# Kernel optimization log

Measured on AMD Instinct MI355X. Metric: run time of the kernel, lower is better.

Reference implementation:

```python
import jax, jax.numpy as jnp
import numpy as np

N_NODES = 100000; N_EDGES = 800000
N_SVC = 51200; E_SVC = 409600
B = 1024; OUT = 50; HID = 128; EMB = 64; VOCAB = 100
BN_EPS = 1e-5


def _bn(x, g, b):
    # BatchNorm1d in training mode: biased batch statistics
    m = x.mean(0)
    v = x.var(0)
    return (x - m) * jax.lax.rsqrt(v + BN_EPS) * g + b


def _gin(x, ei, W1, b1, bng, bnb, W2, b2, eps, n):
    # GINConv: nn((1+eps)*x + sum_{j->i} x_j), aggregate source feats at target ei[1]
    agg = jax.ops.segment_sum(x[ei[0]], ei[1], num_segments=n)
    h = (1.0 + eps) * x + agg
    h = _bn(h @ W1 + b1, bng, bnb)
    return jax.nn.relu(h) @ W2 + b2


def _gcn(x, ei, ew, W, b, n):
    # GCNConv with edge weights: add self loops (w=1), symmetric normalization
    xw = x @ W
    loop = jnp.arange(n)
    row = jnp.concatenate([ei[0], loop])
    col = jnp.concatenate([ei[1], loop])
    w = jnp.concatenate([ew, jnp.ones((n,), ew.dtype)])
    deg = jax.ops.segment_sum(w, col, num_segments=n)
    dinv = jnp.where(deg > 0, jax.lax.rsqrt(deg), 0.0)
    norm = dinv[row] * w * dinv[col]
    return jax.ops.segment_sum(norm[:, None] * xw[row], col, num_segments=n) + b


def setup_inputs() -> dict:
    key = jax.random.key(0)
    ks = jax.random.split(key, 48)
    p = lambda k, s: jax.random.normal(k, s, jnp.float32) * 0.05
    H2 = 2 * HID
    inp = dict(
        node_ids=jax.random.randint(ks[0], (N_NODES,), 0, VOCAB),
        node_feats=jax.random.normal(ks[1], (N_NODES, 6), jnp.float32),
        edge_index=jax.random.randint(ks[2], (2, N_EDGES), 0, N_NODES),
        svc_ids=jax.random.randint(ks[3], (N_SVC,), 0, VOCAB),
        svc_feats=jax.random.normal(ks[4], (N_SVC, 4), jnp.float32),
        edge_index_service=jax.random.randint(ks[5], (2, E_SVC), 0, N_SVC),
        edge_attr_service=jax.random.uniform(ks[6], (E_SVC,), jnp.float32),
        batch=jnp.sort(jax.random.randint(ks[7], (N_NODES,), 0, B)),
        num_graphs=B,
        out_channels=OUT,
        emb_node=p(ks[8], (VOCAB, EMB)),
        emb_svc=p(ks[9], (VOCAB, EMB)),
        # GIN layer 0 (in = EMB + 6)
        g0_W1=p(ks[10], (EMB + 6, H2)), g0_b1=jnp.zeros((H2,), jnp.float32),
        g0_bng1=jnp.ones((H2,), jnp.float32), g0_bnb1=jnp.zeros((H2,), jnp.float32),
        g0_W2=p(ks[11], (H2, HID)), g0_b2=jnp.zeros((HID,), jnp.float32),
        g0_eps=jnp.zeros((), jnp.float32),
        bn0_g=jnp.ones((HID,), jnp.float32), bn0_b=jnp.zeros((HID,), jnp.float32),
        # GIN layer 1 (in = HID)
        g1_W1=p(ks[12], (HID, H2)), g1_b1=jnp.zeros((H2,), jnp.float32),
        g1_bng1=jnp.ones((H2,), jnp.float32), g1_bnb1=jnp.zeros((H2,), jnp.float32),
        g1_W2=p(ks[13], (H2, HID)), g1_b2=jnp.zeros((HID,), jnp.float32),
        g1_eps=jnp.zeros((), jnp.float32),
        bn1_g=jnp.ones((HID,), jnp.float32), bn1_b=jnp.zeros((HID,), jnp.float32),
        node_lin_W=p(ks[14], (HID, HID)), node_lin_b=jnp.zeros((HID,), jnp.float32),
        # GCN layer 0 (in = EMB + 4)
        c0_W=p(ks[15], (EMB + 4, H2)), c0_b=jnp.zeros((H2,), jnp.float32),
        cbn0_g=jnp.ones((H2,), jnp.float32), cbn0_b=jnp.zeros((H2,), jnp.float32),
        # GCN layer 1 (in = 2*HID)
        c1_W=p(ks[16], (H2, H2)), c1_b=jnp.zeros((H2,), jnp.float32),
        cbn1_g=jnp.ones((H2,), jnp.float32), cbn1_b=jnp.zeros((H2,), jnp.float32),
        svc_lin_W=p(ks[17], (H2, HID)), svc_lin_b=jnp.zeros((HID,), jnp.float32),
    )
    return inp


def reference(node_feats, svc_feats, edge_attr_service, emb_node, emb_svc,
              g0_W1, g0_b1, g0_bng1, g0_bnb1, g0_W2, g0_b2, g0_eps, bn0_g, bn0_b,
              g1_W1, g1_b1, g1_bng1, g1_bnb1, g1_W2, g1_b2, g1_eps, bn1_g, bn1_b,
              node_lin_W, node_lin_b,
              c0_W, c0_b, cbn0_g, cbn0_b, c1_W, c1_b, cbn1_g, cbn1_b,
              svc_lin_W, svc_lin_b,
              node_ids, svc_ids, edge_index, edge_index_service, batch,
              num_graphs, out_channels):
    n = node_feats.shape[0]
    ns = svc_feats.shape[0]
    # node branch: embedding(col 0) ++ 6 float cols, 2 GIN layers
    x = jnp.concatenate([emb_node[node_ids], node_feats], axis=-1)
    x = jax.nn.relu(_bn(_gin(x, edge_index, g0_W1, g0_b1, g0_bng1, g0_bnb1,
                             g0_W2, g0_b2, g0_eps, n), bn0_g, bn0_b))
    x = jax.nn.relu(_bn(_gin(x, edge_index, g1_W1, g1_b1, g1_bng1, g1_bnb1,
                             g1_W2, g1_b2, g1_eps, n), bn1_g, bn1_b))
    # service branch: embedding ++ 4 qos cols, 2 GCN layers (isServices=True)
    xs = jnp.concatenate([emb_svc[svc_ids], svc_feats], axis=-1)
    xs = jax.nn.relu(_bn(_gcn(xs, edge_index_service, edge_attr_service, c0_W, c0_b, ns),
                         cbn0_g, cbn0_b))
    xs = jax.nn.relu(_bn(_gcn(xs, edge_index_service, edge_attr_service, c1_W, c1_b, ns),
                         cbn1_g, cbn1_b))
    xs = xs @ svc_lin_W + svc_lin_b
    x = x @ node_lin_W + node_lin_b
    # scatter-mean pooling over graphs
    cnt = jax.ops.segment_sum(jnp.ones((n,), x.dtype), batch, num_segments=num_graphs)
    xg = jax.ops.segment_sum(x, batch, num_segments=num_graphs) / jnp.clip(cnt, 1.0)[:, None]
    # scatter-mean over service slots: indices [0..out-1] repeated per graph
    svc_batch = jnp.tile(jnp.arange(out_channels), ns // out_channels)
    scnt = jax.ops.segment_sum(jnp.ones((ns,), xs.dtype), svc_batch, num_segments=out_channels)
    xsg = jax.ops.segment_sum(xs, svc_batch, num_segments=out_channels) / jnp.clip(scnt, 1.0)[:, None]
    return jax.nn.sigmoid(xg @ xsg.T)
```

## Files before the change

### kernel.cpp

```cpp
#include <hip/hip_runtime.h>
#include <hip/hip_bf16.h>
#include <cstddef>
#include <cstdint>

typedef __hip_bfloat16 bf16;
typedef __attribute__((ext_vector_type(8))) short short8;
typedef __attribute__((ext_vector_type(4))) float floatx4;

static __device__ __forceinline__ float b2f(bf16 v) { return __bfloat162float(v); }

static __device__ __forceinline__ short f2bf(float f) {
    unsigned u = __float_as_uint(f);
    unsigned r = u + 0x7FFF + ((u >> 16) & 1);
    return (short)(r >> 16);
}
static __device__ __forceinline__ float bf2f(short h) {
    return __uint_as_float(((unsigned)(unsigned short)h) << 16);
}
static __device__ __forceinline__ float loadf(const void* p, int mode, size_t i) {
    if (mode == 1) return b2f(((const bf16*)p)[i]);
    if (mode == 2) return ((const float*)p)[i];
    return 0.f;
}

#define NCONV 35
struct DetArgs { const void* src[NCONV]; int n[NCONV]; };

__global__ void detect_all(DetArgs a, int* __restrict__ modes) {
    int b = blockIdx.x;
    int n = a.n[b];
    const unsigned short* w = (const unsigned short*)a.src[b];
    __shared__ int cz, cbad, cevz, codz;
    if (threadIdx.x == 0) { cz = 0; cbad = 0; cevz = 0; codz = 0; }
    __syncthreads();
    int K = n < 2048 ? n : 2048;
    int z = 0, bad = 0, evz = 0, odz = 0;
    for (int i = threadIdx.x; i < K; i += blockDim.x) {
        unsigned short v = w[i];
        int e = (v >> 7) & 0xFF;
        bool isz = (v & 0x7FFF) == 0;
        if (isz) { z++; if (i & 1) odz++; else evz++; }
        else if (e < 91 || e > 140) bad++;
    }
    atomicAdd(&cz, z); atomicAdd(&cbad, bad);
    atomicAdd(&cevz, evz); atomicAdd(&codz, odz);
    __syncthreads();
    if (threadIdx.x == 0) {
        int mode;
        if (cz >= K) mode = 0;
        else if (cbad * 16 > K) mode = 2;
        else if (cevz * 4 > K && codz * 16 < K) mode = 2;
        else mode = 1;
        modes[b] = mode;
    }
}

struct WtArgs {
    const void* W[8]; short* wt[8];
    int midx[8]; int KW[8]; int ldw[8]; int Kpad[8]; int N[8];
};
__global__ void wt_build_all(WtArgs a, const int* __restrict__ modes) {
    int e = blockIdx.y;
    int n = blockIdx.x; if (n >= a.N[e]) return;
    int k = threadIdx.x; if (k >= a.Kpad[e]) return;
    float v = (k < a.KW[e]) ? loadf(a.W[e], modes[a.midx[e]], (size_t)k * a.ldw[e] + n) : 0.f;
    a.wt[e][(size_t)n * a.Kpad[e] + k] = f2bf(v);
}

__global__ void build_feat_bf16(const void* __restrict__ emb, const int* __restrict__ ids,
                                const void* __restrict__ feats, const int* __restrict__ modes,
                                int eidx, int fidx, unsigned short* __restrict__ P,
                                int nf, int Ws) {
    int i = blockIdx.x;
    int d = threadIdx.x;
    if (d >= Ws) return;
    float v;
    if (d < 64)           v = loadf(emb, modes[eidx], (size_t)ids[i] * 64 + d);
    else if (d < 64 + nf) v = loadf(feats, modes[fidx], (size_t)i * nf + (d - 64));
    else                  v = 0.f;
    P[(size_t)i * Ws + d] = (unsigned short)f2bf(v);
}

__global__ void csr_count(const int* __restrict__ dst, int nE, int* __restrict__ cnt) {
    int e = blockIdx.x * blockDim.x + threadIdx.x;
    if (e < nE) atomicAdd(&cnt[dst[e]], 1);
}

__global__ __launch_bounds__(256) void scan_part(const int* __restrict__ cnt, int n,
                                                 int* __restrict__ bsum) {
    __shared__ int red[256];
    int blk = blockIdx.x, t = threadIdx.x;
    int base = blk * 1024 + t * 4;
    int s = 0;
    #pragma unroll
    for (int k = 0; k < 4; ++k) { int i = base + k; if (i < n) s += cnt[i]; }
    red[t] = s;
    __syncthreads();
    for (int off = 128; off > 0; off >>= 1) {
        if (t < off) red[t] += red[t + off];
        __syncthreads();
    }
    if (t == 0) bsum[blk] = red[0];
}

__global__ __launch_bounds__(128) void scan_mid(int* __restrict__ bsum, int nb,
                                                int* __restrict__ rowptr, int n) {
    __shared__ int sh[128];
    int t = threadIdx.x;
    int v = (t < nb) ? bsum[t] : 0;
    sh[t] = v;
    __syncthreads();
    for (int off = 1; off < 128; off <<= 1) {
        int u = (t >= off) ? sh[t - off] : 0;
        __syncthreads();
        sh[t] += u;
        __syncthreads();
    }
    if (t < nb) bsum[t] = sh[t] - v;
    if (t == 127) rowptr[n] = sh[127];
}

__global__ __launch_bounds__(256) void scan_fin(const int* __restrict__ cnt, int n,
                                                const int* __restrict__ bsum,
                                                int* __restrict__ rowptr, int* __restrict__ cursor) {
    __shared__ int sh[256];
    int blk = blockIdx.x, t = threadIdx.x;
    int base = blk * 1024 + t * 4;
    int v[4], s = 0;
    #pragma unroll
    for (int k = 0; k < 4; ++k) { int i = base + k; v[k] = (i < n) ? cnt[i] : 0; s += v[k]; }
    sh[t] = s;
    __syncthreads();
    for (int off = 1; off < 256; off <<= 1) {
        int u = (t >= off) ? sh[t - off] : 0;
        __syncthreads();
        sh[t] += u;
        __syncthreads();
    }
    int run = sh[t] - s + bsum[blk];
    #pragma unroll
    for (int k = 0; k < 4; ++k) {
        int i = base + k;
        if (i < n) { rowptr[i] = run; cursor[i] = run; run += v[k]; }
    }
}

__global__ void csr_fill(const int* __restrict__ src, const int* __restrict__ dst,
                         const void* __restrict__ w, const int* __restrict__ modes, int widx,
                         const float* __restrict__ dinv, int nE, int* __restrict__ cursor,
                         int* __restrict__ adj, short* __restrict__ adjw) {
    int e = blockIdx.x * blockDim.x + threadIdx.x;
    if (e < nE) {
        int s = src[e];
        int pos = atomicAdd(&cursor[dst[e]], 1);
        adj[pos] = s;
        if (adjw) adjw[pos] = f2bf(dinv[s] * loadf(w, modes[widx], e));
    }
}

__global__ __launch_bounds__(256) void gin_gather_bf16(
        const unsigned short* __restrict__ P, const int* __restrict__ rowptr,
        const int* __restrict__ adj, const void* __restrict__ eps,
        const int* __restrict__ modes, int eidx,
        const float* __restrict__ bnsc, const float* __restrict__ bnsh,
        unsigned short* __restrict__ Po, int Ws, int nN) {
    int W8 = Ws >> 3;
    int g = threadIdx.x >> 4;
    int l = threadIdx.x & 15;
    int i = blockIdx.x * 16 + g;
    if (i >= nN || l >= W8) return;
    float epsv = 1.0f + loadf(eps, modes[eidx], 0);
    float sc[8], sh[8];
    bool bn = bnsc != nullptr;
    if (bn) {
        *(float4*)&sc[0] = *(const float4*)(bnsc + l * 8);
        *(float4*)&sc[4] = *(const float4*)(bnsc + l * 8 + 4);
        *(float4*)&sh[0] = *(const float4*)(bnsh + l * 8);
        *(float4*)&sh[4] = *(const float4*)(bnsh + l * 8 + 4);
    }
    int lo = rowptr[i], hi = rowptr[i + 1];
    float acc[8] = {};
    for (int p = lo; p < hi; ++p) {
        short8 v = *(const short8*)(P + (size_t)adj[p] * Ws + l * 8);
        #pragma unroll
        for (int j = 0; j < 8; ++j) {
            float y = bf2f(v[j]);
            if (bn) y = fmaxf(fmaf(y, sc[j], sh[j]), 0.f);
            acc[j] += y;
        }
    }
    size_t o = (size_t)i * Ws + l * 8;
    short8 sv = *(const short8*)(P + o);
    short8 r;
    #pragma unroll
    for (int j = 0; j < 8; ++j) {
        float y = bf2f(sv[j]);
        if (bn) y = fmaxf(fmaf(y, sc[j], sh[j]), 0.f);
        r[j] = f2bf(acc[j] + epsv * y);
    }
    *(short8*)(Po + o) = r;
}

__global__ __launch_bounds__(256) void gcn_gather_bf16(
        const unsigned short* __restrict__ xw, const int* __restrict__ rowptr,
        const int* __restrict__ adj, const short* __restrict__ adjw,
        const float* __restrict__ dinv, const void* __restrict__ bias,
        const int* __restrict__ modes, int bidx, float* __restrict__ out, int nS) {
    int g = threadIdx.x >> 5;
    int l = threadIdx.x & 31;
    int i = blockIdx.x * 8 + g;
    if (i >= nS) return;
    float di = dinv[i];
    int bmode = modes[bidx];
    size_t o = (size_t)i * 256 + l * 8;
    short8 sv = *(const short8*)(xw + o);
    float dd = di * di;
    float acc[8];
    #pragma unroll
    for (int j = 0; j < 8; ++j)
        acc[j] = bf2f(sv[j]) * dd + loadf(bias, bmode, l * 8 + j);
    int lo = rowptr[i], hi = rowptr[i + 1];
    for (int p = lo; p < hi; ++p) {
        float w = di * bf2f(adjw[p]);
        short8 v = *(const short8*)(xw + (size_t)adj[p] * 256 + l * 8);
        #pragma unroll
        for (int j = 0; j < 8; ++j)
            acc[j] += w * bf2f(v[j]);
    }
    *(float4*)(out + o) = *(float4*)&acc[0];
    *(float4*)(out + o + 4) = *(float4*)&acc[4];
}

__global__ __launch_bounds__(256) void gemm_mfma(
        const void* __restrict__ A, int afmt, int ldk,
        const float* __restrict__ bnsc, const float* __restrict__ bnsh,
        const short* __restrict__ Wt,
        const void* __restrict__ bias, const int* __restrict__ modes, int bias_midx,
        float* __restrict__ outF, unsigned short* __restrict__ oB,
        float* __restrict__ stats, int M, int N, int ksteps, int omode) {
    int tid  = threadIdx.x;
    int wv   = tid >> 6, lane = tid & 63;
    int m16  = lane & 15, q = lane >> 4;
    int bm   = blockIdx.y * 128 + wv * 32;
    int n0   = blockIdx.x * 128;
    int r0 = min(bm + m16, M - 1);
    int r1 = min(bm + 16 + m16, M - 1);
    const short8* ba0 = (const short8*)((const short*)A + (size_t)r0 * ldk + q * 8);
    const short8* ba1 = (const short8*)((const short*)A + (size_t)r1 * ldk + q * 8);
    const float*  fa0 = (const float*)A + (size_t)r0 * ldk + q * 8;
    const float*  fa1 = (const float*)A + (size_t)r1 * ldk + q * 8;
    const short8* pb[8];
    #pragma unroll
    for (int nt = 0; nt < 8; ++nt)
        pb[nt] = (const short8*)(Wt + (size_t)(n0 + nt * 16 + m16) * ldk + q * 8);

    floatx4 acc[2][8];
    #pragma unroll
    for (int mt = 0; mt < 2; ++mt)
        #pragma unroll
        for (int nt = 0; nt < 8; ++nt)
            acc[mt][nt] = (floatx4){0.f, 0.f, 0.f, 0.f};

    bool bn = bnsc != nullptr;
    for (int ks = 0; ks < ksteps; ++ks) {
        int idx = ks * 4;
        short8 a0, a1;
        if (afmt == 0 && !bn) {
            a0 = ba0[idx];
            a1 = ba1[idx];
        } else {
            float v0[8], v1[8];
            if (afmt == 0) {
                short8 u0 = ba0[idx], u1 = ba1[idx];
                #pragma unroll
                for (int j = 0; j < 8; ++j) { v0[j] = bf2f(u0[j]); v1[j] = bf2f(u1[j]); }
            } else {
                *(float4*)&v0[0] = *(const float4*)(fa0 + ks * 32);
                *(float4*)&v0[4] = *(const float4*)(fa0 + ks * 32 + 4);
                *(float4*)&v1[0] = *(const float4*)(fa1 + ks * 32);
                *(float4*)&v1[4] = *(const float4*)(fa1 + ks * 32 + 4);
            }
            if (bn) {
                int c0 = ks * 32 + q * 8;
                float scv[8], shv[8];
                *(float4*)&scv[0] = *(const float4*)(bnsc + c0);
                *(float4*)&scv[4] = *(const float4*)(bnsc + c0 + 4);
                *(float4*)&shv[0] = *(const float4*)(bnsh + c0);
                *(float4*)&shv[4] = *(const float4*)(bnsh + c0 + 4);
                #pragma unroll
                for (int j = 0; j < 8; ++j) {
                    v0[j] = fmaxf(fmaf(v0[j], scv[j], shv[j]), 0.f);
                    v1[j] = fmaxf(fmaf(v1[j], scv[j], shv[j]), 0.f);
                }
            }
            #pragma unroll
            for (int j = 0; j < 8; ++j) { a0[j] = f2bf(v0[j]); a1[j] = f2bf(v1[j]); }
        }
        #pragma unroll
        for (int nt = 0; nt < 8; ++nt) {
            short8 b = pb[nt][idx];
            acc[0][nt] = __builtin_amdgcn_mfma_f32_16x16x32_bf16(a0, b, acc[0][nt], 0, 0, 0);
            acc[1][nt] = __builtin_amdgcn_mfma_f32_16x16x32_bf16(a1, b, acc[1][nt], 0, 0, 0);
        }
    }

    float bv[8];
    int bmode = bias ? modes[bias_midx] : 0;
    #pragma unroll
    for (int nt = 0; nt < 8; ++nt)
        bv[nt] = bias ? loadf(bias, bmode, n0 + nt * 16 + m16) : 0.f;

    if (omode) {
        __shared__ unsigned short tile[128][136];
        __shared__ float redS[4][128], redQ[4][128];
        float sA[8], qA[8];
        #pragma unroll
        for (int nt = 0; nt < 8; ++nt) { sA[nt] = 0.f; qA[nt] = 0.f; }
        #pragma unroll
        for (int mt = 0; mt < 2; ++mt)
            #pragma unroll
            for (int r = 0; r < 4; ++r) {
                int rl = wv * 32 + mt * 16 + q * 4 + r;
                bool ok = (bm + mt * 16 + q * 4 + r) < M;
                #pragma unroll
                for (int nt = 0; nt < 8; ++nt) {
                    float v = acc[mt][nt][r] + bv[nt];
                    tile[rl][nt * 16 + m16] = (unsigned short)f2bf(v);
                    if (ok && omode == 1) { sA[nt] += v; qA[nt] += v * v; }
                }
            }
        if (omode == 1) {
            #pragma unroll
            for (int nt = 0; nt < 8; ++nt) {
                sA[nt] += __shfl_xor(sA[nt], 16); sA[nt] += __shfl_xor(sA[nt], 32);
                qA[nt] += __shfl_xor(qA[nt], 16); qA[nt] += __shfl_xor(qA[nt], 32);
            }
            if (q == 0) {
                #pragma unroll
                for (int nt = 0; nt < 8; ++nt) {
                    redS[wv][nt * 16 + m16] = sA[nt];
                    redQ[wv][nt * 16 + m16] = qA[nt];
                }
            }
        }
        __syncthreads();
        int rb = blockIdx.y * 128;
        #pragma unroll
        for (int c = 0; c < 8; ++c) {
            int lin = c * 256 + tid;
            int row = lin >> 4;
            int cu  = lin & 15;
            int grow = rb + row;
            if (grow < M)
                *(short8*)(oB + (size_t)grow * N + n0 + cu * 8) = *(short8*)&tile[row][cu * 8];
        }
        if (omode == 1 && tid < 128) {
            float s = 0.f, qq = 0.f;
            #pragma unroll
            for (int w = 0; w < 4; ++w) { s += redS[w][tid]; qq += redQ[w][tid]; }
            atomicAdd(&stats[n0 + tid], s);
            atomicAdd(&stats[N + n0 + tid], qq);
        }
    } else {
        #pragma unroll
        for (int mt = 0; mt < 2; ++mt)
            #pragma unroll
            for (int r = 0; r < 4; ++r) {
                int row = bm + mt * 16 + q * 4 + r;
                if (row >= M) continue;
                #pragma unroll
                for (int nt = 0; nt < 8; ++nt)
                    outF[(size_t)row * N + n0 + nt * 16 + m16] = acc[mt][nt][r] + bv[nt];
            }
    }
}

__global__ void bn_finalize(float* __restrict__ stats, const void* __restrict__ g,
                            const void* __restrict__ b, const int* __restrict__ modes,
                            int gidx, int bidx, int C, float invM) {
    int c = threadIdx.x;
    if (c < C) {
        float mean = stats[c] * invM;
        float var  = fmaxf(stats[C + c] * invM - mean * mean, 0.f);
        float sc   = loadf(g, modes[gidx], c) * rsqrtf(var + 1e-5f);
        stats[2 * C + c] = sc;
        stats[3 * C + c] = loadf(b, modes[bidx], c) - mean * sc;
    }
}

__global__ void bn_stats_f32(const float* __restrict__ X, float* __restrict__ stats,
                             int M, int C, int rows) {
    int c = threadIdx.x;
    int r0 = blockIdx.x * rows;
    int r1 = min(r0 + rows, M);
    float s = 0.f, s2 = 0.f;
    for (int r = r0; r < r1; ++r) {
        float v = X[(size_t)r * C + c];
        s += v; s2 += v * v;
    }
    atomicAdd(&stats[c], s);
    atomicAdd(&stats[C + c], s2);
}

__global__ void deg_scatter(const void* __restrict__ ew, const int* __restrict__ modes, int eidx,
                            const int* __restrict__ col, float* __restrict__ deg, int nE) {
    int e = blockIdx.x * blockDim.x + threadIdx.x;
    if (e < nE) atomicAdd(&deg[col[e]], loadf(ew, modes[eidx], e));
}

__global__ void dinv_fin(float* __restrict__ deg, int n) {
    int i = blockIdx.x * blockDim.x + threadIdx.x;
    if (i < n) {
        float d = deg[i] + 1.0f;
        deg[i] = d > 0.f ? rsqrtf(d) : 0.f;
    }
}

__global__ void pool_sorted_bf16(const unsigned short* __restrict__ xn,
                                 const int* __restrict__ batch,
                                 float* __restrict__ xg, int nN) {
    int g = blockIdx.x;
    int lo = 0, hi = nN;
    while (lo < hi) { int mid = (lo + hi) >> 1; if (batch[mid] < g) lo = mid + 1; else hi = mid; }
    int lo2 = lo, hi2 = nN;
    while (lo2 < hi2) { int mid = (lo2 + hi2) >> 1; if (batch[mid] < g + 1) lo2 = mid + 1; else hi2 = mid; }
    int d = threadIdx.x;
    float s = 0.f;
    for (int r = lo; r < lo2; ++r) s += bf2f((short)xn[(size_t)r * 128 + d]);
    xg[(size_t)g * 128 + d] = s / fmaxf((float)(lo2 - lo), 1.0f);
}

__global__ void svc_pool1(const float* __restrict__ xsl, float* __restrict__ partial) {
    int o = blockIdx.x;
    int c = blockIdx.y;
    int d = threadIdx.x;
    float s = 0.f;
    int r0 = c * 128;
    for (int r = r0; r < r0 + 128; ++r)
        s += xsl[((size_t)(r * 50 + o)) * 128 + d];
    partial[((size_t)(o * 8 + c)) * 128 + d] = s;
}

__global__ void svc_pool2(const float* __restrict__ partial, float* __restrict__ xsg) {
    int o = blockIdx.x;
    int d = threadIdx.x;
    float s = 0.f;
    #pragma unroll
    for (int c = 0; c < 8; ++c)
        s += partial[((size_t)(o * 8 + c)) * 128 + d];
    xsg[o * 128 + d] = s * (1.0f / 1024.0f);
}

__global__ void final_out(const float* __restrict__ xg, const float* __restrict__ xsg,
                          const int* __restrict__ modes, void* __restrict__ out) {
    __shared__ float xrow[128];
    int g = blockIdx.x;
    for (int d = threadIdx.x; d < 128; d += 64) xrow[d] = xg[(size_t)g * 128 + d];
    __syncthreads();
    int o = threadIdx.x;
    if (o < 50) {
        const float* xs = xsg + o * 128;
        float s = 0.f;
        #pragma unroll 4
        for (int d = 0; d < 128; ++d) s += xrow[d] * xs[d];
        float sg = 1.0f / (1.0f + __expf(-s));
        if (modes[0] == 1) ((bf16*)out)[(size_t)g * 50 + o] = __float2bfloat16(sg);
        else               ((float*)out)[(size_t)g * 50 + o] = sg;
    }
}

extern "C" void kernel_launch(void* const* d_in, const int* in_sizes, int n_in,
                              void* d_out, int out_size, void* d_ws, size_t ws_size,
                              hipStream_t stream) {
    const int nN = 100000, nE = 800000, nS = 51200, nES = 409600;
    const int Bg = 1024;

    const int* node_ids = (const int*)d_in[0];
    const int* ei       = (const int*)d_in[2];
    const int* svc_ids  = (const int*)d_in[3];
    const int* eis      = (const int*)d_in[5];
    const int* batch    = (const int*)d_in[7];

    float* ws    = (float*)d_ws;
    int*   modes = (int*)ws;
    float* stats = ws + 64;
    float* dinv  = ws + 1088;
    float* xsg   = ws + 52288;
    int*   bsum  = (int*)(ws + 58688);
    int*   rp_n  = (int*)(ws + 58944);
    int*   adj_n = (int*)(ws + 158948);
    int*   rp_s  = (int*)(ws + 958948);
    int*   adj_s = (int*)(ws + 1010152);
    short* adw_s = (short*)(ws + 1419752);
    short* wtb   = (short*)(ws + 1624552);
    float* xg    = ws + 1755624;
    float* part  = ws + 1886696;
    float* A25   = ws + 1937896;
    float* B13   = ws + 27537896;
    float* C13   = ws + 40645096;
    size_t need  = (size_t)53752296 * 4;
    if (ws_size < need) return;
    int* cur_n = (int*)xg;
    int* cur_s = (int*)part;
    int* bsum_n = bsum;
    int* bsum_s = bsum + 128;

    unsigned short* A25B = (unsigned short*)A25;
    unsigned short* B13B = (unsigned short*)B13;
    unsigned short* C13B = (unsigned short*)C13;
    float* B13F = B13;  float* A25F = A25;

    float* sc256 = stats + 512; float* sh256 = stats + 768;
    float* sc128 = stats + 256; float* sh128 = stats + 384;

    short* wt0 = wtb;
    short* wt1 = wt0 + 24576;
    short* wt2 = wt1 + 32768;
    short* wt3 = wt2 + 32768;
    short* wt4 = wt3 + 32768;
    short* wt5 = wt4 + 16384;
    short* wt6 = wt5 + 24576;
    short* wt7 = wt6 + 65536;

    static const int conv_idx[NCONV] = {1, 4, 6, 10, 11,
        12, 13, 14, 15, 16, 17, 18, 19, 20,
        21, 22, 23, 24, 25, 26, 27, 28, 29,
        30, 31, 32, 33, 34, 35, 36, 37, 38, 39, 40, 41};
    DetArgs da;
    for (int b = 0; b < NCONV; ++b) { da.src[b] = d_in[conv_idx[b]]; da.n[b] = in_sizes[conv_idx[b]]; }
    detect_all<<<NCONV, 256, 0, stream>>>(da, modes);

    {
        WtArgs wa;
        const int din_i[8]  = {12, 16, 21, 25, 30, 32, 36, 40};
        const int midx_i[8] = {5, 9, 14, 18, 23, 25, 29, 33};
        const int KW_i[8]   = {70, 256, 128, 256, 128, 68, 256, 256};
        const int ldw_i[8]  = {256, 128, 256, 128, 128, 256, 256, 128};
        short* wt_i[8]      = {wt0, wt1, wt2, wt3, wt4, wt5, wt6, wt7};
        const int Kp_i[8]   = {96, 256, 128, 256, 128, 96, 256, 256};
        const int N_i[8]    = {256, 128, 256, 128, 128, 256, 256, 128};
        for (int e = 0; e < 8; ++e) {
            wa.W[e] = d_in[din_i[e]]; wa.midx[e] = midx_i[e]; wa.KW[e] = KW_i[e];
            wa.ldw[e] = ldw_i[e]; wa.wt[e] = wt_i[e]; wa.Kpad[e] = Kp_i[e]; wa.N[e] = N_i[e];
        }
        wt_build_all<<<dim3(256, 8), 256, 0, stream>>>(wa, modes);
    }

    hipMemsetAsync(dinv, 0, nS * sizeof(float), stream);
    deg_scatter<<<(nES + 255) / 256, 256, 0, stream>>>(d_in[6], modes, 2, eis + nES, dinv, nES);
    dinv_fin<<<(nS + 255) / 256, 256, 0, stream>>>(dinv, nS);

    const int nbN = (nN + 1023) / 1024, nbS = (nS + 1023) / 1024;
    hipMemsetAsync(cur_n, 0, nN * sizeof(int), stream);
    csr_count<<<(nE + 255) / 256, 256, 0, stream>>>(ei + nE, nE, cur_n);
    scan_part<<<nbN, 256, 0, stream>>>(cur_n, nN, bsum_n);
    scan_mid<<<1, 128, 0, stream>>>(bsum_n, nbN, rp_n, nN);
    scan_fin<<<nbN, 256, 0, stream>>>(cur_n, nN, bsum_n, rp_n, cur_n);
    csr_fill<<<(nE + 255) / 256, 256, 0, stream>>>(ei, ei + nE, nullptr, modes, 2, nullptr,
                                                   nE, cur_n, adj_n, nullptr);

    hipMemsetAsync(cur_s, 0, nS * sizeof(int), stream);
    csr_count<<<(nES + 255) / 256, 256, 0, stream>>>(eis + nES, nES, cur_s);
    scan_part<<<nbS, 256, 0, stream>>>(cur_s, nS, bsum_s);
    scan_mid<<<1, 128, 0, stream>>>(bsum_s, nbS, rp_s, nS);
    scan_fin<<<nbS, 256, 0, stream>>>(cur_s, nS, bsum_s, rp_s, cur_s);
    csr_fill<<<(nES + 255) / 256, 256, 0, stream>>>(eis, eis + nES, d_in[6], modes, 2, dinv,
                                                    nES, cur_s, adj_s, adw_s);

    auto gemm = [&](const void* A, int afmt, int ldk, const float* bsc, const float* bsh,
                    const short* Wt, const void* bias, int bidx,
                    float* outF, unsigned short* oB, int M, int N, int om) {
        if (om == 1) hipMemsetAsync(stats, 0, 2 * N * sizeof(float), stream);
        dim3 grid(N / 128, (M + 127) / 128);
        gemm_mfma<<<grid, 256, 0, stream>>>(A, afmt, ldk, bsc, bsh, Wt, bias, modes, bidx,
                                            outF, oB, stats, M, N, ldk / 32, om);
    };
    auto bnfin = [&](int gidx, int bidx, const void* g, const void* b, int C, int M) {
        bn_finalize<<<1, C, 0, stream>>>(stats, g, b, modes, gidx, bidx, C, 1.0f / M);
    };

    build_feat_bf16<<<nN, 128, 0, stream>>>(d_in[10], node_ids, d_in[1], modes, 3, 0,
                                            C13B, 6, 96);
    gin_gather_bf16<<<(nN + 15) / 16, 256, 0, stream>>>(C13B, rp_n, adj_n, d_in[18], modes, 11,
                                                        nullptr, nullptr, B13B, 96, nN);
    gemm(B13B, 0, 96, nullptr, nullptr, wt0, d_in[13], 6, nullptr, A25B, nN, 256, 1);
    bnfin(7, 8, d_in[14], d_in[15], 256, nN);
    gemm(A25B, 0, 256, sc256, sh256, wt1, d_in[17], 10, nullptr, C13B, nN, 128, 1);
    bnfin(12, 13, d_in[19], d_in[20], 128, nN);
    gin_gather_bf16<<<(nN + 15) / 16, 256, 0, stream>>>(C13B, rp_n, adj_n, d_in[27], modes, 20,
                                                        sc128, sh128, B13B, 128, nN);
    gemm(B13B, 0, 128, nullptr, nullptr, wt2, d_in[22], 15, nullptr, A25B, nN, 256, 1);
    bnfin(16, 17, d_in[23], d_in[24], 256, nN);
    gemm(A25B, 0, 256, sc256, sh256, wt3, d_in[26], 19, nullptr, C13B, nN, 128, 1);
    bnfin(21, 22, d_in[28], d_in[29], 128, nN);
    gemm(C13B, 0, 128, sc128, sh128, wt4, d_in[31], 24, nullptr, B13B, nN, 128, 2);
    pool_sorted_bf16<<<Bg, 128, 0, stream>>>(B13B, batch, xg, nN);

    build_feat_bf16<<<nS, 128, 0, stream>>>(d_in[11], svc_ids, d_in[4], modes, 4, 1,
                                            C13B, 4, 96);
    gemm(C13B, 0, 96, nullptr, nullptr, wt5, nullptr, 0, nullptr, B13B, nS, 256, 2);
    gcn_gather_bf16<<<(nS + 7) / 8, 256, 0, stream>>>(B13B, rp_s, adj_s, adw_s, dinv, d_in[33],
                                                      modes, 26, A25F, nS);
    hipMemsetAsync(stats, 0, 2 * 256 * sizeof(float), stream);
    bn_stats_f32<<<(nS + 31) / 32, 256, 0, stream>>>(A25F, stats, nS, 256, 32);
    bnfin(27, 28, d_in[34], d_in[35], 256, nS);
    gemm(A25F, 1, 256, sc256, sh256, wt6, nullptr, 0, nullptr, B13B, nS, 256, 2);
    gcn_gather_bf16<<<(nS + 7) / 8, 256, 0, stream>>>(B13B, rp_s, adj_s, adw_s, dinv, d_in[37],
                                                      modes, 30, A25F, nS);
    hipMemsetAsync(stats, 0, 2 * 256 * sizeof(float), stream);
    bn_stats_f32<<<(nS + 31) / 32, 256, 0, stream>>>(A25F, stats, nS, 256, 32);
    bnfin(31, 32, d_in[38], d_in[39], 256, nS);
    gemm(A25F, 1, 256, sc256, sh256, wt7, d_in[41], 34, B13F, nullptr, nS, 128, 0);
    svc_pool1<<<dim3(50, 8), 128, 0, stream>>>(B13F, part);
    svc_pool2<<<50, 128, 0, stream>>>(part, xsg);

    final_out<<<Bg, 64, 0, stream>>>(xg, xsg, modes, d_out);
}
```

Baseline: 1.107 ms.

## Stage A tiles through LDS with coalesced loads and halve GEMM row tile

The MFMA GEMM now loads the A operand cooperatively, row-coalesced, into a shared-memory slab of 64 rows by up to 128 columns. The BN-affine, ReLU and bf16 conversion are applied once during staging, and waves then read their MFMA fragments from LDS instead of doing strided per-lane global loads. The row tile shrinks from 128 to 64 (one 16-row M tile per wave), which doubles the grid and the number of blocks sharing each B column. The epilogue reuses the same LDS buffer. In exchange it adds two barriers per slab, reduces MFMA work per B load, and re-reads weights across twice as many blocks.

Measured after the change: 1.295 ms. +17.0%, slower.

```diff
diff --git a/kernel.cpp b/kernel.cpp
--- a/kernel.cpp
+++ b/kernel.cpp
@@ -237,71 +237,74 @@
         const short* __restrict__ Wt,
         const void* __restrict__ bias, const int* __restrict__ modes, int bias_midx,
         float* __restrict__ outF, unsigned short* __restrict__ oB,
-        float* __restrict__ stats, int M, int N, int ksteps, int omode) {
+        float* __restrict__ stats, int M, int N, int omode) {
+    __shared__ unsigned short sbuf[64][132];
+    __shared__ float redS[4][128], redQ[4][128];
     int tid  = threadIdx.x;
     int wv   = tid >> 6, lane = tid & 63;
     int m16  = lane & 15, q = lane >> 4;
-    int bm   = blockIdx.y * 128 + wv * 32;
+    int bm   = blockIdx.y * 64;
     int n0   = blockIdx.x * 128;
-    int r0 = min(bm + m16, M - 1);
-    int r1 = min(bm + 16 + m16, M - 1);
-    const short8* ba0 = (const short8*)((const short*)A + (size_t)r0 * ldk + q * 8);
-    const short8* ba1 = (const short8*)((const short*)A + (size_t)r1 * ldk + q * 8);
-    const float*  fa0 = (const float*)A + (size_t)r0 * ldk + q * 8;
-    const float*  fa1 = (const float*)A + (size_t)r1 * ldk + q * 8;
+
     const short8* pb[8];
     #pragma unroll
     for (int nt = 0; nt < 8; ++nt)
         pb[nt] = (const short8*)(Wt + (size_t)(n0 + nt * 16 + m16) * ldk + q * 8);
 
-    floatx4 acc[2][8];
-    #pragma unroll
-    for (int mt = 0; mt < 2; ++mt)
-        #pragma unroll
-        for (int nt = 0; nt < 8; ++nt)
-            acc[mt][nt] = (floatx4){0.f, 0.f, 0.f, 0.f};
+    floatx4 acc[8];
+    #pragma unroll
+    for (int nt = 0; nt < 8; ++nt)
+        acc[nt] = (floatx4){0.f, 0.f, 0.f, 0.f};
 
     bool bn = bnsc != nullptr;
-    for (int ks = 0; ks < ksteps; ++ks) {
-        int idx = ks * 4;
-        short8 a0, a1;
-        if (afmt == 0 && !bn) {
-            a0 = ba0[idx];
-            a1 = ba1[idx];
-        } else {
-            float v0[8], v1[8];
-            if (afmt == 0) {
-                short8 u0 = ba0[idx], u1 = ba1[idx];
+    int nslab = (ldk + 127) >> 7;
+    for (int s = 0; s < nslab; ++s) {
+        int W   = min(128, ldk - s * 128);
+        int W16 = W >> 3;
+        int units = 64 * W16;
+        for (int u = tid; u < units; u += 256) {
+            int row = u / W16, cu = u - row * W16;
+            int grow = min(bm + row, M - 1);
+            int gcol = s * 128 + cu * 8;
+            short8 val;
+            if (afmt == 0 && !bn) {
+                val = *(const short8*)((const short*)A + (size_t)grow * ldk + gcol);
+            } else {
+                float v[8];
+                if (afmt == 0) {
+                    short8 uv = *(const short8*)((const short*)A + (size_t)grow * ldk + gcol);
+                    #pragma unroll
+                    for (int j = 0; j < 8; ++j) v[j] = bf2f(uv[j]);
+                } else {
+                    const float* fp = (const float*)A + (size_t)grow * ldk + gcol;
+                    *(float4*)&v[0] = *(const float4*)fp;
+                    *(float4*)&v[4] = *(const float4*)(fp + 4);
+                }
+                if (bn) {
+                    float scv[8], shv[8];
+                    *(float4*)&scv[0] = *(const float4*)(bnsc + gcol);
+                    *(float4*)&scv[4] = *(const float4*)(bnsc + gcol + 4);
+                    *(float4*)&shv[0] = *(const float4*)(bnsh + gcol);
+                    *(float4*)&shv[4] = *(const float4*)(bnsh + gcol + 4);
+                    #pragma unroll
+                    for (int j = 0; j < 8; ++j)
+                        v[j] = fmaxf(fmaf(v[j], scv[j], shv[j]), 0.f);
+                }
                 #pragma unroll
-                for (int j = 0; j < 8; ++j) { v0[j] = bf2f(u0[j]); v1[j] = bf2f(u1[j]); }
-            } else {
-                *(float4*)&v0[0] = *(const float4*)(fa0 + ks * 32);
-                *(float4*)&v0[4] = *(const float4*)(fa0 + ks * 32 + 4);
-                *(float4*)&v1[0] = *(const float4*)(fa1 + ks * 32);
-                *(float4*)&v1[4] = *(const float4*)(fa1 + ks * 32 + 4);
+                for (int j = 0; j < 8; ++j) val[j] = f2bf(v[j]);
             }
-            if (bn) {
-                int c0 = ks * 32 + q * 8;
-                float scv[8], shv[8];
-                *(float4*)&scv[0] = *(const float4*)(bnsc + c0);
-                *(float4*)&scv[4] = *(const float4*)(bnsc + c0 + 4);
-                *(float4*)&shv[0] = *(const float4*)(bnsh + c0);
-                *(float4*)&shv[4] = *(const float4*)(bnsh + c0 + 4);
-                #pragma unroll
-                for (int j = 0; j < 8; ++j) {
-                    v0[j] = fmaxf(fmaf(v0[j], scv[j], shv[j]), 0.f);
-                    v1[j] = fmaxf(fmaf(v1[j], scv[j], shv[j]), 0.f);
-                }
-            }
+            *(short8*)&sbuf[row][cu * 8] = val;
+        }
+        __syncthreads();
+        int kst = W >> 5;
+        for (int ks = 0; ks < kst; ++ks) {
+            short8 a = *(const short8*)&sbuf[wv * 16 + m16][ks * 32 + q * 8];
+            int bi = s * 16 + ks * 4;
             #pragma unroll
-            for (int j = 0; j < 8; ++j) { a0[j] = f2bf(v0[j]); a1[j] = f2bf(v1[j]); }
-        }
-        #pragma unroll
-        for (int nt = 0; nt < 8; ++nt) {
-            short8 b = pb[nt][idx];
-            acc[0][nt] = __builtin_amdgcn_mfma_f32_16x16x32_bf16(a0, b, acc[0][nt], 0, 0, 0);
-            acc[1][nt] = __builtin_amdgcn_mfma_f32_16x16x32_bf16(a1, b, acc[1][nt], 0, 0, 0);
-        }
+            for (int nt = 0; nt < 8; ++nt)
+                acc[nt] = __builtin_amdgcn_mfma_f32_16x16x32_bf16(a, pb[nt][bi], acc[nt], 0, 0, 0);
+        }
+        __syncthreads();
     }
 
     float bv[8];
@@ -311,24 +314,20 @@
         bv[nt] = bias ? loadf(bias, bmode, n0 + nt * 16 + m16) : 0.f;
 
     if (omode) {
-        __shared__ unsigned short tile[128][136];
-        __shared__ float redS[4][128], redQ[4][128];
         float sA[8], qA[8];
         #pragma unroll
         for (int nt = 0; nt < 8; ++nt) { sA[nt] = 0.f; qA[nt] = 0.f; }
         #pragma unroll
-        for (int mt = 0; mt < 2; ++mt)
+        for (int r = 0; r < 4; ++r) {
+            int rl = wv * 16 + q * 4 + r;
+            bool ok = (bm + rl) < M;
             #pragma unroll
-            for (int r = 0; r < 4; ++r) {
-                int rl = wv * 32 + mt * 16 + q * 4 + r;
-                bool ok = (bm + mt * 16 + q * 4 + r) < M;
-                #pragma unroll
-                for (int nt = 0; nt < 8; ++nt) {
-                    float v = acc[mt][nt][r] + bv[nt];
-                    tile[rl][nt * 16 + m16] = (unsigned short)f2bf(v);
-                    if (ok && omode == 1) { sA[nt] += v; qA[nt] += v * v; }
-                }
+            for (int nt = 0; nt < 8; ++nt) {
+                float v = acc[nt][r] + bv[nt];
+                sbuf[rl][nt * 16 + m16] = (unsigned short)f2bf(v);
+                if (ok && omode == 1) { sA[nt] += v; qA[nt] += v * v; }
             }
+        }
         if (omode == 1) {
             #pragma unroll
             for (int nt = 0; nt < 8; ++nt) {
@@ -344,15 +343,14 @@
             }
         }
         __syncthreads();
-        int rb = blockIdx.y * 128;
         #pragma unroll
-        for (int c = 0; c < 8; ++c) {
+        for (int c = 0; c < 4; ++c) {
             int lin = c * 256 + tid;
             int row = lin >> 4;
             int cu  = lin & 15;
-            int grow = rb + row;
+            int grow = bm + row;
             if (grow < M)
-                *(short8*)(oB + (size_t)grow * N + n0 + cu * 8) = *(short8*)&tile[row][cu * 8];
+                *(short8*)(oB + (size_t)grow * N + n0 + cu * 8) = *(short8*)&sbuf[row][cu * 8];
         }
         if (omode == 1 && tid < 128) {
             float s = 0.f, qq = 0.f;
@@ -363,15 +361,13 @@
         }
     } else {
         #pragma unroll
-        for (int mt = 0; mt < 2; ++mt)
+        for (int r = 0; r < 4; ++r) {
+            int row = bm + wv * 16 + q * 4 + r;
+            if (row >= M) continue;
             #pragma unroll
-            for (int r = 0; r < 4; ++r) {
-                int row = bm + mt * 16 + q * 4 + r;
-                if (row >= M) continue;
-                #pragma unroll
-                for (int nt = 0; nt < 8; ++nt)
-                    outF[(size_t)row * N + n0 + nt * 16 + m16] = acc[mt][nt][r] + bv[nt];
-            }
+            for (int nt = 0; nt < 8; ++nt)
+                outF[(size_t)row * N + n0 + nt * 16 + m16] = acc[nt][r] + bv[nt];
+        }
     }
 }
 
@@ -571,9 +567,9 @@
                     const short* Wt, const void* bias, int bidx,
                     float* outF, unsigned short* oB, int M, int N, int om) {
         if (om == 1) hipMemsetAsync(stats, 0, 2 * N * sizeof(float), stream);
-        dim3 grid(N / 128, (M + 127) / 128);
+        dim3 grid(N / 128, (M + 63) / 64);
         gemm_mfma<<<grid, 256, 0, stream>>>(A, afmt, ldk, bsc, bsh, Wt, bias, modes, bidx,
-                                            outF, oB, stats, M, N, ldk / 32, om);
+                                            outF, oB, stats, M, N, om);
     };
     auto bnfin = [&](int gidx, int bidx, const void* g, const void* b, int C, int M) {
         bn_finalize<<<1, C, 0, stream>>>(stats, g, b, modes, gidx, bidx, C, 1.0f / M);
```
